# Kernel optimization log

Measured on AMD Instinct MI355X. Metric: run time of the kernel, lower is better.

## Reference

```python
import jax, jax.numpy as jnp
import numpy as np

N = 50000        # nodes
E = 800000       # edges (avg degree 16)
HID = 96         # hidden_channels
HEADS = 4        # heads passed to SRGATConv
D = HID // HEADS # per-head dim
R = 38           # num_relations
NEG_SLOPE = 0.2  # LeakyReLU slope for attention logits


def setup_inputs() -> dict:
    key = jax.random.key(0)
    ks = jax.random.split(key, 9)
    x = jax.random.normal(ks[0], (N, HID), jnp.float32)
    edge_index = jax.random.randint(ks[1], (2, E), 0, N, dtype=jnp.int32)
    edge_type = jax.random.randint(ks[2], (E,), 0, R, dtype=jnp.int32)
    s = 1.0 / np.sqrt(HID)
    W = jax.random.normal(ks[3], (HID, HID), jnp.float32) * s          # node projection
    rel_emb = jax.random.normal(ks[4], (R, HID), jnp.float32) * s      # relation embeddings
    att_src = jax.random.normal(ks[5], (HEADS, D), jnp.float32) * 0.1  # attention vectors
    att_dst = jax.random.normal(ks[6], (HEADS, D), jnp.float32) * 0.1
    att_rel = jax.random.normal(ks[7], (HEADS, D), jnp.float32) * 0.1
    bias = jnp.zeros((HID,), jnp.float32)
    return {"x": x, "edge_index": edge_index, "edge_type": edge_type,
            "W": W, "rel_emb": rel_emb, "att_src": att_src,
            "att_dst": att_dst, "att_rel": att_rel, "bias": bias}


def reference(x, edge_index, edge_type, W, rel_emb, att_src, att_dst, att_rel, bias):
    # SRGATConv: relation-aware multi-head graph attention, then GELU wrapper.
    n = x.shape[0]
    src, dst = edge_index[0], edge_index[1]
    h = (x @ W).reshape(n, HEADS, D)                    # [N,H,D]
    r = rel_emb[edge_type].reshape(-1, HEADS, D)        # [E,H,D] gathered relation feats
    h_src = h[src]                                      # [E,H,D] irregular gather
    h_dst = h[dst]
    # attention logits per edge/head
    logits = ((h_src * att_src).sum(-1)
              + (h_dst * att_dst).sum(-1)
              + (r * att_rel).sum(-1))                  # [E,H]
    logits = jax.nn.leaky_relu(logits, NEG_SLOPE)
    # segment softmax over incoming edges of each destination node
    lmax = jax.ops.segment_max(logits, dst, num_segments=n)   # [N,H]
    e = jnp.exp(logits - lmax[dst])
    denom = jax.ops.segment_sum(e, dst, num_segments=n)       # [N,H]
    alpha = e / denom[dst]                                    # [E,H]
    # weighted message scatter
    msg = alpha[:, :, None] * (h_src + r)                     # [E,H,D]
    out = jax.ops.segment_sum(msg, dst, num_segments=n).reshape(n, HID) + bias
    out = jax.nn.gelu(out)
    return out, alpha
```

## Files before the change

### kernel.cpp

```cpp
#include <hip/hip_runtime.h>
#include <hip/hip_fp16.h>
#include <math.h>

#define HIDC 96
#define HEADS 4
#define DH 24
#define RMAX 40
#define CAP 56
#define DEGS 8

__device__ __forceinline__ __half2 u2h2(unsigned u) {
    return *reinterpret_cast<__half2*>(&u);
}
__device__ __forceinline__ unsigned h22u(__half2 h) {
    return *reinterpret_cast<unsigned*>(&h);
}

__global__ __launch_bounds__(192) void gemm96(const float* __restrict__ x,
                                              const float* __restrict__ W,
                                              __half* __restrict__ h16,
                                              int* __restrict__ deg, int n) {
    for (int i = blockIdx.x * 192 + threadIdx.x; i < n * DEGS; i += gridDim.x * 192)
        deg[i] = 0;

    __shared__ float Ws[HIDC * HIDC];
    __shared__ float xs[32 * HIDC];
    for (int i = threadIdx.x; i < HIDC * HIDC / 4; i += 192)
        reinterpret_cast<float4*>(Ws)[i] = reinterpret_cast<const float4*>(W)[i];
    int c4 = threadIdx.x % 24;
    int r0 = (threadIdx.x / 24) * 4;
    const float4* xs4 = reinterpret_cast<const float4*>(xs);
    const float4* Ws4 = reinterpret_cast<const float4*>(Ws);
    uint2* h8 = reinterpret_cast<uint2*>(h16);
    int numTiles = (n + 31) >> 5;
    for (int tile = blockIdx.x; tile < numTiles; tile += gridDim.x) {
        int row0 = tile << 5;
        int rows = min(32, n - row0);
        __syncthreads();
        for (int i = threadIdx.x; i < rows * 24; i += 192)
            reinterpret_cast<float4*>(xs)[i] =
                reinterpret_cast<const float4*>(x + (size_t)row0 * HIDC)[i];
        __syncthreads();
        float4 acc[4];
#pragma unroll
        for (int i = 0; i < 4; ++i) acc[i] = make_float4(0.f, 0.f, 0.f, 0.f);
#pragma unroll 4
        for (int k4 = 0; k4 < 24; ++k4) {
            float4 xv[4], wv[4];
#pragma unroll
            for (int i = 0; i < 4; ++i) xv[i] = xs4[(r0 + i) * 24 + k4];
#pragma unroll
            for (int j = 0; j < 4; ++j) wv[j] = Ws4[(k4 * 4 + j) * 24 + c4];
#pragma unroll
            for (int i = 0; i < 4; ++i) {
                const float xi[4] = {xv[i].x, xv[i].y, xv[i].z, xv[i].w};
#pragma unroll
                for (int j = 0; j < 4; ++j) {
                    acc[i].x = fmaf(xi[j], wv[j].x, acc[i].x);
                    acc[i].y = fmaf(xi[j], wv[j].y, acc[i].y);
                    acc[i].z = fmaf(xi[j], wv[j].z, acc[i].z);
                    acc[i].w = fmaf(xi[j], wv[j].w, acc[i].w);
                }
            }
        }
#pragma unroll
        for (int i = 0; i < 4; ++i)
            if (r0 + i < rows) {
                __half2 lo = __floats2half2_rn(acc[i].x, acc[i].y);
                __half2 hi = __floats2half2_rn(acc[i].z, acc[i].w);
                uint2 pk;
                pk.x = h22u(lo);
                pk.y = h22u(hi);
                h8[(size_t)(row0 + r0 + i) * 24 + c4] = pk;
            }
    }
}

__global__ __launch_bounds__(256) void node_dots(
    const __half* __restrict__ h16,
    const float* __restrict__ att_src, const float* __restrict__ att_dst,
    const float* __restrict__ rel, const float* __restrict__ att_rel,
    float4* __restrict__ ps, float* __restrict__ pdi,
    float4* __restrict__ pr, int n, int R_) {
    if (blockIdx.x == gridDim.x - 1) {
        int t = threadIdx.x;
        if (t < R_) {
            const float4* rp = reinterpret_cast<const float4*>(rel + (size_t)t * HIDC);
            const float4* ar = reinterpret_cast<const float4*>(att_rel);
            float acc[HEADS] = {0, 0, 0, 0};
#pragma unroll
            for (int c = 0; c < 24; ++c) {
                float4 v = rp[c], a = ar[c];
                acc[c / 6] += v.x * a.x + v.y * a.y + v.z * a.z + v.w * a.w;
            }
            pr[t] = make_float4(acc[0], acc[1], acc[2], acc[3]);
        }
        return;
    }
    int i = blockIdx.x * blockDim.x + threadIdx.x;
    if (i >= n) return;
    const uint2* hp = reinterpret_cast<const uint2*>(h16 + (size_t)i * HIDC);
    const float4* as = reinterpret_cast<const float4*>(att_src);
    const float4* ad = reinterpret_cast<const float4*>(att_dst);
    float accs[HEADS] = {0, 0, 0, 0}, accd[HEADS] = {0, 0, 0, 0};
#pragma unroll
    for (int c = 0; c < 24; ++c) {
        uint2 hv = hp[c];
        float2 f0 = __half22float2(u2h2(hv.x));
        float2 f1 = __half22float2(u2h2(hv.y));
        float4 a = as[c], d = ad[c];
        int hh = c / 6;
        accs[hh] += f0.x * a.x + f0.y * a.y + f1.x * a.z + f1.y * a.w;
        accd[hh] += f0.x * d.x + f0.y * d.y + f1.x * d.z + f1.y * d.w;
    }
    ps[i] = make_float4(accs[0], accs[1], accs[2], accs[3]);
    *reinterpret_cast<float4*>(pdi + (size_t)i * 8) =
        make_float4(accd[0], accd[1], accd[2], accd[3]);
}

__device__ __forceinline__ float4 ev4(float4 a, float4 b, float4 c) {
    float l0 = a.x + b.x + c.x, l1 = a.y + b.y + c.y;
    float l2 = a.z + b.z + c.z, l3 = a.w + b.w + c.w;
    l0 = l0 >= 0.f ? l0 : 0.2f * l0;
    l1 = l1 >= 0.f ? l1 : 0.2f * l1;
    l2 = l2 >= 0.f ? l2 : 0.2f * l2;
    l3 = l3 >= 0.f ? l3 : 0.2f * l3;
    return make_float4(__expf(l0), __expf(l1), __expf(l2), __expf(l3));
}

__device__ __forceinline__ float gelu_f(float v) {
    float u = 0.7978845608028654f * (v + 0.044715f * v * v * v);
    u = fminf(fmaxf(u, -15.f), 15.f);
    float t = __expf(2.f * u);
    return 0.5f * v * (1.f + (t - 1.f) / (t + 1.f));
}

__global__ void fill_bucket(const int* __restrict__ src, const int* __restrict__ dst,
                            const int* __restrict__ et,
                            const float4* __restrict__ ps, const float* __restrict__ pdi,
                            const float4* __restrict__ pr,
                            int* __restrict__ deg, int4* __restrict__ bucket, int E_) {
    int e = blockIdx.x * blockDim.x + threadIdx.x;
    if (e >= E_) return;
    int d = dst[e];
    int pos = atomicAdd(&deg[(size_t)d * DEGS], 1);
    if (pos < CAP) {
        int s = src[e], t = et[e];
        float4 b = *reinterpret_cast<const float4*>(pdi + (size_t)d * 8);
        float4 v = ev4(ps[s], b, pr[t]);
        int4 pk;
        pk.x = s;
        pk.y = t;
        pk.z = (int)h22u(__floats2half2_rn(v.x, v.y));
        pk.w = (int)h22u(__floats2half2_rn(v.z, v.w));
        bucket[(size_t)d * CAP + pos] = pk;
    }
}

__global__ __launch_bounds__(256) void node_agg(
    const __half* __restrict__ h16, const float* __restrict__ rel,
    const int4* __restrict__ bucket, const int* __restrict__ deg,
    float* __restrict__ pdi, const float* __restrict__ bias,
    float* __restrict__ out, int n, int R_) {
    __shared__ unsigned short relh[RMAX * HIDC];
    for (int i = threadIdx.x; i < R_ * 24; i += 256) {
        float4 v = reinterpret_cast<const float4*>(rel)[i];
        uint2 pk;
        pk.x = h22u(__floats2half2_rn(v.x, v.y));
        pk.y = h22u(__floats2half2_rn(v.z, v.w));
        reinterpret_cast<uint2*>(relh)[i] = pk;
    }
    __syncthreads();

    int lane = threadIdx.x & 31;
    if (lane >= 24) return;
    const int j = lane;
    const int j4 = 4 * j;
    const int hh = j / 6;
    const float4 bv = *reinterpret_cast<const float4*>(bias + j4);
    const uint2* relr = reinterpret_cast<const uint2*>(relh);

    int hw0 = (blockIdx.x * blockDim.x + threadIdx.x) >> 5;
    int nHW = (gridDim.x * blockDim.x) >> 5;

    for (int hw = hw0; hw < n; hw += nHW) {
        int cnt = min(deg[(size_t)hw * DEGS], CAP);
        const int4* sp = bucket + (size_t)hw * CAP;
        float a0 = 0.f, a1 = 0.f, a2 = 0.f, a3 = 0.f;
        float dsum = 0.f;

        if (cnt > 0) {
            const int lim = cnt - 1;
            int4 pc[4];
#pragma unroll
            for (int u = 0; u < 4; ++u) pc[u] = sp[min(u, lim)];

            for (int k = 0; k < cnt; k += 4) {
                uint2 hv[4];
#pragma unroll
                for (int u = 0; u < 4; ++u)
                    hv[u] = *reinterpret_cast<const uint2*>(
                        h16 + (size_t)pc[u].x * HIDC + j4);
                int4 pn[4];
#pragma unroll
                for (int u = 0; u < 4; ++u) pn[u] = sp[min(k + 4 + u, lim)];
#pragma unroll
                for (int u = 0; u < 4; ++u) {
                    unsigned w = (hh & 2) ? (unsigned)pc[u].w : (unsigned)pc[u].z;
                    unsigned bits16 = (hh & 1) ? (w >> 16) : (w & 0xffffu);
                    float e = __half2float(__low2half(u2h2(bits16)));
                    e = (k + u < cnt) ? e : 0.f;
                    dsum += e;
                    uint2 rv = relr[pc[u].y * 24 + j];
                    float2 f01 = __half22float2(__hadd2(u2h2(hv[u].x), u2h2(rv.x)));
                    float2 f23 = __half22float2(__hadd2(u2h2(hv[u].y), u2h2(rv.y)));
                    a0 = fmaf(e, f01.x, a0);
                    a1 = fmaf(e, f01.y, a1);
                    a2 = fmaf(e, f23.x, a2);
                    a3 = fmaf(e, f23.y, a3);
                }
#pragma unroll
                for (int u = 0; u < 4; ++u) pc[u] = pn[u];
            }
        }
        float inv = dsum > 0.f ? 1.f / dsum : 0.f;
        if ((j % 6) == 0) pdi[(size_t)hw * 8 + 4 + hh] = inv;
        float4 o;
        o.x = gelu_f(a0 * inv + bv.x);
        o.y = gelu_f(a1 * inv + bv.y);
        o.z = gelu_f(a2 * inv + bv.z);
        o.w = gelu_f(a3 * inv + bv.w);
        *reinterpret_cast<float4*>(out + (size_t)hw * HIDC + j4) = o;
    }
}

__global__ void alpha_edge(const int* __restrict__ src, const int* __restrict__ dst,
                           const int* __restrict__ et,
                           const float4* __restrict__ ps, const float* __restrict__ pdi,
                           const float4* __restrict__ pr,
                           float4* __restrict__ alpha, int E_) {
    int e = blockIdx.x * blockDim.x + threadIdx.x;
    if (e >= E_) return;
    int d = dst[e];
    const float4* rec = reinterpret_cast<const float4*>(pdi + (size_t)d * 8);
    float4 b = rec[0];
    float4 iv = rec[1];
    float4 v = ev4(ps[src[e]], b, pr[et[e]]);
    alpha[e] = make_float4(v.x * iv.x, v.y * iv.y, v.z * iv.z, v.w * iv.w);
}

extern "C" void kernel_launch(void* const* d_in, const int* in_sizes, int n_in,
                              void* d_out, int out_size, void* d_ws, size_t ws_size,
                              hipStream_t stream) {
    const float* x       = (const float*)d_in[0];
    const int*   eidx    = (const int*)d_in[1];
    const int*   etype   = (const int*)d_in[2];
    const float* W       = (const float*)d_in[3];
    const float* rel     = (const float*)d_in[4];
    const float* att_src = (const float*)d_in[5];
    const float* att_dst = (const float*)d_in[6];
    const float* att_rel = (const float*)d_in[7];
    const float* bias    = (const float*)d_in[8];

    int N_ = in_sizes[0] / HIDC;
    int E_ = in_sizes[1] / 2;
    int R_ = in_sizes[4] / HIDC;
    const int* src  = eidx;
    const int* dstp = eidx + E_;

    char* ws = (char*)d_ws;
    __half* h16    = (__half*)ws;  ws += (size_t)N_ * HIDC * 2;
    float4* ps     = (float4*)ws;  ws += (size_t)N_ * 16;
    float*  pdi    = (float*)ws;   ws += (size_t)N_ * 32;
    float4* pr     = (float4*)ws;  ws += 1024;
    int*    deg    = (int*)ws;     ws += (size_t)N_ * DEGS * 4;
    int4*   bucket = (int4*)ws;    ws += (size_t)N_ * CAP * 16;

    float*  outv  = (float*)d_out;
    float4* alpha = (float4*)(outv + (size_t)N_ * HIDC);

    gemm96<<<(N_ + 31) / 32, 192, 0, stream>>>(x, W, h16, deg, N_);

    node_dots<<<(N_ + 255) / 256 + 1, 256, 0, stream>>>(
        h16, att_src, att_dst, rel, att_rel, ps, pdi, pr, N_, R_);

    fill_bucket<<<(E_ + 255) / 256, 256, 0, stream>>>(
        src, dstp, etype, ps, pdi, pr, deg, bucket, E_);

    node_agg<<<2048, 256, 0, stream>>>(
        h16, rel, bucket, deg, pdi, bias, outv, N_, R_);

    alpha_edge<<<(E_ + 255) / 256, 256, 0, stream>>>(
        src, dstp, etype, ps, pdi, pr, alpha, E_);
}
```

Baseline: 213.5 us.

## Fuse node dots with bucket fill and recompute edge logits in aggregation

```diff
diff --git a/kernel.cpp b/kernel.cpp
--- a/kernel.cpp
+++ b/kernel.cpp
@@ -6,8 +6,10 @@
 #define HEADS 4
 #define DH 24
 #define RMAX 40
-#define CAP 56
+#define CAP 64
 #define DEGS 8
+#define SRCB 18
+#define SRCM ((1 << SRCB) - 1)
 
 __device__ __forceinline__ __half2 u2h2(unsigned u) {
     return *reinterpret_cast<__half2*>(&u);
@@ -76,13 +78,37 @@
     }
 }
 
-__global__ __launch_bounds__(256) void node_dots(
+__global__ __launch_bounds__(256) void nd_fill(
     const __half* __restrict__ h16,
     const float* __restrict__ att_src, const float* __restrict__ att_dst,
     const float* __restrict__ rel, const float* __restrict__ att_rel,
-    float4* __restrict__ ps, float* __restrict__ pdi,
-    float4* __restrict__ pr, int n, int R_) {
-    if (blockIdx.x == gridDim.x - 1) {
+    float4* __restrict__ ps, float* __restrict__ pdi, float4* __restrict__ pr,
+    const int* __restrict__ src, const int* __restrict__ dst,
+    const int* __restrict__ et,
+    int* __restrict__ deg, int* __restrict__ bucket,
+    int n, int R_, int E_, int nB) {
+    int bid = blockIdx.x;
+    if (bid < nB) {
+        int i = bid * 256 + threadIdx.x;
+        if (i >= n) return;
+        const uint2* hp = reinterpret_cast<const uint2*>(h16 + (size_t)i * HIDC);
+        const float4* as = reinterpret_cast<const float4*>(att_src);
+        const float4* ad = reinterpret_cast<const float4*>(att_dst);
+        float accs[HEADS] = {0, 0, 0, 0}, accd[HEADS] = {0, 0, 0, 0};
+#pragma unroll
+        for (int c = 0; c < 24; ++c) {
+            uint2 hv = hp[c];
+            float2 f0 = __half22float2(u2h2(hv.x));
+            float2 f1 = __half22float2(u2h2(hv.y));
+            float4 a = as[c], d = ad[c];
+            int hh = c / 6;
+            accs[hh] += f0.x * a.x + f0.y * a.y + f1.x * a.z + f1.y * a.w;
+            accd[hh] += f0.x * d.x + f0.y * d.y + f1.x * d.z + f1.y * d.w;
+        }
+        ps[i] = make_float4(accs[0], accs[1], accs[2], accs[3]);
+        *reinterpret_cast<float4*>(pdi + (size_t)i * 8) =
+            make_float4(accd[0], accd[1], accd[2], accd[3]);
+    } else if (bid == nB) {
         int t = threadIdx.x;
         if (t < R_) {
             const float4* rp = reinterpret_cast<const float4*>(rel + (size_t)t * HIDC);
@@ -95,27 +121,14 @@
             }
             pr[t] = make_float4(acc[0], acc[1], acc[2], acc[3]);
         }
-        return;
-    }
-    int i = blockIdx.x * blockDim.x + threadIdx.x;
-    if (i >= n) return;
-    const uint2* hp = reinterpret_cast<const uint2*>(h16 + (size_t)i * HIDC);
-    const float4* as = reinterpret_cast<const float4*>(att_src);
-    const float4* ad = reinterpret_cast<const float4*>(att_dst);
-    float accs[HEADS] = {0, 0, 0, 0}, accd[HEADS] = {0, 0, 0, 0};
-#pragma unroll
-    for (int c = 0; c < 24; ++c) {
-        uint2 hv = hp[c];
-        float2 f0 = __half22float2(u2h2(hv.x));
-        float2 f1 = __half22float2(u2h2(hv.y));
-        float4 a = as[c], d = ad[c];
-        int hh = c / 6;
-        accs[hh] += f0.x * a.x + f0.y * a.y + f1.x * a.z + f1.y * a.w;
-        accd[hh] += f0.x * d.x + f0.y * d.y + f1.x * d.z + f1.y * d.w;
-    }
-    ps[i] = make_float4(accs[0], accs[1], accs[2], accs[3]);
-    *reinterpret_cast<float4*>(pdi + (size_t)i * 8) =
-        make_float4(accd[0], accd[1], accd[2], accd[3]);
+    } else {
+        int e = (bid - nB - 1) * 256 + threadIdx.x;
+        if (e >= E_) return;
+        int d = dst[e];
+        int pos = atomicAdd(&deg[(size_t)d * DEGS], 1);
+        if (pos < CAP)
+            bucket[(size_t)d * CAP + pos] = src[e] | (et[e] << SRCB);
+    }
 }
 
 __device__ __forceinline__ float4 ev4(float4 a, float4 b, float4 c) {
@@ -135,40 +148,25 @@
     return 0.5f * v * (1.f + (t - 1.f) / (t + 1.f));
 }
 
-__global__ void fill_bucket(const int* __restrict__ src, const int* __restrict__ dst,
-                            const int* __restrict__ et,
-                            const float4* __restrict__ ps, const float* __restrict__ pdi,
-                            const float4* __restrict__ pr,
-                            int* __restrict__ deg, int4* __restrict__ bucket, int E_) {
-    int e = blockIdx.x * blockDim.x + threadIdx.x;
-    if (e >= E_) return;
-    int d = dst[e];
-    int pos = atomicAdd(&deg[(size_t)d * DEGS], 1);
-    if (pos < CAP) {
-        int s = src[e], t = et[e];
-        float4 b = *reinterpret_cast<const float4*>(pdi + (size_t)d * 8);
-        float4 v = ev4(ps[s], b, pr[t]);
-        int4 pk;
-        pk.x = s;
-        pk.y = t;
-        pk.z = (int)h22u(__floats2half2_rn(v.x, v.y));
-        pk.w = (int)h22u(__floats2half2_rn(v.z, v.w));
-        bucket[(size_t)d * CAP + pos] = pk;
-    }
-}
-
 __global__ __launch_bounds__(256) void node_agg(
     const __half* __restrict__ h16, const float* __restrict__ rel,
-    const int4* __restrict__ bucket, const int* __restrict__ deg,
-    float* __restrict__ pdi, const float* __restrict__ bias,
+    const int* __restrict__ bucket, const int* __restrict__ deg,
+    const float* __restrict__ ps1, float* __restrict__ pdi,
+    const float4* __restrict__ prg, const float* __restrict__ bias,
     float* __restrict__ out, int n, int R_) {
     __shared__ unsigned short relh[RMAX * HIDC];
+    __shared__ float prs4[RMAX * 4];
     for (int i = threadIdx.x; i < R_ * 24; i += 256) {
         float4 v = reinterpret_cast<const float4*>(rel)[i];
         uint2 pk;
         pk.x = h22u(__floats2half2_rn(v.x, v.y));
         pk.y = h22u(__floats2half2_rn(v.z, v.w));
         reinterpret_cast<uint2*>(relh)[i] = pk;
+    }
+    for (int i = threadIdx.x; i < R_; i += 256) {
+        float4 v = prg[i];
+        prs4[4 * i + 0] = v.x; prs4[4 * i + 1] = v.y;
+        prs4[4 * i + 2] = v.z; prs4[4 * i + 3] = v.w;
     }
     __syncthreads();
 
@@ -185,33 +183,40 @@
 
     for (int hw = hw0; hw < n; hw += nHW) {
         int cnt = min(deg[(size_t)hw * DEGS], CAP);
-        const int4* sp = bucket + (size_t)hw * CAP;
+        const int* spw = bucket + (size_t)hw * CAP;
+        float pdh = pdi[(size_t)hw * 8 + hh];
         float a0 = 0.f, a1 = 0.f, a2 = 0.f, a3 = 0.f;
         float dsum = 0.f;
 
         if (cnt > 0) {
             const int lim = cnt - 1;
-            int4 pc[4];
-#pragma unroll
-            for (int u = 0; u < 4; ++u) pc[u] = sp[min(u, lim)];
+            int wc[4];
+#pragma unroll
+            for (int u = 0; u < 4; ++u) wc[u] = spw[min(u, lim)];
 
             for (int k = 0; k < cnt; k += 4) {
+                int s[4], t[4];
+#pragma unroll
+                for (int u = 0; u < 4; ++u) { s[u] = wc[u] & SRCM; t[u] = wc[u] >> SRCB; }
                 uint2 hv[4];
+                float pv[4];
 #pragma unroll
                 for (int u = 0; u < 4; ++u)
                     hv[u] = *reinterpret_cast<const uint2*>(
-                        h16 + (size_t)pc[u].x * HIDC + j4);
-                int4 pn[4];
-#pragma unroll
-                for (int u = 0; u < 4; ++u) pn[u] = sp[min(k + 4 + u, lim)];
+                        h16 + (size_t)s[u] * HIDC + j4);
+#pragma unroll
+                for (int u = 0; u < 4; ++u) pv[u] = ps1[(size_t)s[u] * 4 + hh];
+                int wn[4];
+#pragma unroll
+                for (int u = 0; u < 4; ++u) wn[u] = spw[min(k + 4 + u, lim)];
 #pragma unroll
                 for (int u = 0; u < 4; ++u) {
-                    unsigned w = (hh & 2) ? (unsigned)pc[u].w : (unsigned)pc[u].z;
-                    unsigned bits16 = (hh & 1) ? (w >> 16) : (w & 0xffffu);
-                    float e = __half2float(__low2half(u2h2(bits16)));
+                    float l = pv[u] + pdh + prs4[t[u] * 4 + hh];
+                    l = l >= 0.f ? l : 0.2f * l;
+                    float e = __expf(l);
                     e = (k + u < cnt) ? e : 0.f;
                     dsum += e;
-                    uint2 rv = relr[pc[u].y * 24 + j];
+                    uint2 rv = relr[t[u] * 24 + j];
                     float2 f01 = __half22float2(__hadd2(u2h2(hv[u].x), u2h2(rv.x)));
                     float2 f23 = __half22float2(__hadd2(u2h2(hv[u].y), u2h2(rv.y)));
                     a0 = fmaf(e, f01.x, a0);
@@ -220,7 +225,7 @@
                     a3 = fmaf(e, f23.y, a3);
                 }
 #pragma unroll
-                for (int u = 0; u < 4; ++u) pc[u] = pn[u];
+                for (int u = 0; u < 4; ++u) wc[u] = wn[u];
             }
         }
         float inv = dsum > 0.f ? 1.f / dsum : 0.f;
@@ -274,21 +279,21 @@
     float*  pdi    = (float*)ws;   ws += (size_t)N_ * 32;
     float4* pr     = (float4*)ws;  ws += 1024;
     int*    deg    = (int*)ws;     ws += (size_t)N_ * DEGS * 4;
-    int4*   bucket = (int4*)ws;    ws += (size_t)N_ * CAP * 16;
+    int*    bucket = (int*)ws;     ws += (size_t)N_ * CAP * 4;
 
     float*  outv  = (float*)d_out;
     float4* alpha = (float4*)(outv + (size_t)N_ * HIDC);
 
     gemm96<<<(N_ + 31) / 32, 192, 0, stream>>>(x, W, h16, deg, N_);
 
-    node_dots<<<(N_ + 255) / 256 + 1, 256, 0, stream>>>(
-        h16, att_src, att_dst, rel, att_rel, ps, pdi, pr, N_, R_);
-
-    fill_bucket<<<(E_ + 255) / 256, 256, 0, stream>>>(
-        src, dstp, etype, ps, pdi, pr, deg, bucket, E_);
+    int nB = (N_ + 255) / 256;
+    int eB = (E_ + 255) / 256;
+    nd_fill<<<nB + 1 + eB, 256, 0, stream>>>(
+        h16, att_src, att_dst, rel, att_rel, ps, pdi, pr,
+        src, dstp, etype, deg, bucket, N_, R_, E_, nB);
 
     node_agg<<<2048, 256, 0, stream>>>(
-        h16, rel, bucket, deg, pdi, bias, outv, N_, R_);
+        h16, rel, bucket, deg, (const float*)ps, pdi, pr, bias, outv, N_, R_);
 
     alpha_edge<<<(E_ + 255) / 256, 256, 0, stream>>>(
         src, dstp, etype, ps, pdi, pr, alpha, E_);
```

New measurement: 224.6 us. 5.2% more time.

## Replace per-node atomic bucket fill with two-pass binned counting sort into CSR

Applied to the files above, without the earlier changes.

```diff
diff --git a/kernel.cpp b/kernel.cpp
--- a/kernel.cpp
+++ b/kernel.cpp
@@ -4,10 +4,13 @@
 
 #define HIDC 96
 #define HEADS 4
-#define DH 24
 #define RMAX 40
-#define CAP 56
-#define DEGS 8
+#define BINSZ 128
+#define BINCAP 2560
+#define TILE 2048
+#define SRCB 18
+#define SRCM ((1 << SRCB) - 1)
+#define ETB 6
 
 __device__ __forceinline__ __half2 u2h2(unsigned u) {
     return *reinterpret_cast<__half2*>(&u);
@@ -19,9 +22,10 @@
 __global__ __launch_bounds__(192) void gemm96(const float* __restrict__ x,
                                               const float* __restrict__ W,
                                               __half* __restrict__ h16,
-                                              int* __restrict__ deg, int n) {
-    for (int i = blockIdx.x * 192 + threadIdx.x; i < n * DEGS; i += gridDim.x * 192)
-        deg[i] = 0;
+                                              int* __restrict__ bincnt,
+                                              int n, int nbins) {
+    for (int i = blockIdx.x * 192 + threadIdx.x; i < nbins; i += gridDim.x * 192)
+        bincnt[i] = 0;
 
     __shared__ float Ws[HIDC * HIDC];
     __shared__ float xs[32 * HIDC];
@@ -135,31 +139,120 @@
     return 0.5f * v * (1.f + (t - 1.f) / (t + 1.f));
 }
 
-__global__ void fill_bucket(const int* __restrict__ src, const int* __restrict__ dst,
-                            const int* __restrict__ et,
-                            const float4* __restrict__ ps, const float* __restrict__ pdi,
-                            const float4* __restrict__ pr,
-                            int* __restrict__ deg, int4* __restrict__ bucket, int E_) {
-    int e = blockIdx.x * blockDim.x + threadIdx.x;
-    if (e >= E_) return;
-    int d = dst[e];
-    int pos = atomicAdd(&deg[(size_t)d * DEGS], 1);
-    if (pos < CAP) {
-        int s = src[e], t = et[e];
-        float4 b = *reinterpret_cast<const float4*>(pdi + (size_t)d * 8);
-        float4 v = ev4(ps[s], b, pr[t]);
-        int4 pk;
-        pk.x = s;
-        pk.y = t;
-        pk.z = (int)h22u(__floats2half2_rn(v.x, v.y));
-        pk.w = (int)h22u(__floats2half2_rn(v.z, v.w));
-        bucket[(size_t)d * CAP + pos] = pk;
+__global__ __launch_bounds__(256) void bin_edges(
+    const int* __restrict__ src, const int* __restrict__ dst,
+    const int* __restrict__ et,
+    int* __restrict__ bincnt, int* __restrict__ binwords,
+    int E_, int nbins) {
+    __shared__ int hist[512];
+    __shared__ int base[512];
+    int e0 = blockIdx.x * TILE;
+    for (int i = threadIdx.x; i < nbins; i += 256) hist[i] = 0;
+    __syncthreads();
+    int mybin[8], myrank[8], myword[8];
+#pragma unroll
+    for (int u = 0; u < 8; ++u) {
+        int e = e0 + u * 256 + threadIdx.x;
+        mybin[u] = -1;
+        if (e < E_) {
+            int d = dst[e];
+            int b = d >> 7;
+            myword[u] = src[e] | (et[e] << SRCB) | ((d & (BINSZ - 1)) << (SRCB + ETB));
+            mybin[u] = b;
+            myrank[u] = atomicAdd(&hist[b], 1);
+        }
+    }
+    __syncthreads();
+    for (int i = threadIdx.x; i < nbins; i += 256)
+        base[i] = hist[i] > 0 ? atomicAdd(&bincnt[i], hist[i]) : 0;
+    __syncthreads();
+#pragma unroll
+    for (int u = 0; u < 8; ++u) {
+        if (mybin[u] >= 0) {
+            int pos = base[mybin[u]] + myrank[u];
+            if (pos < BINCAP)
+                binwords[(size_t)mybin[u] * BINCAP + pos] = myword[u];
+        }
+    }
+}
+
+__global__ __launch_bounds__(256) void bin_sort(
+    const int* __restrict__ bincnt, const int* __restrict__ binwords,
+    const float4* __restrict__ ps, const float* __restrict__ pdi,
+    const float4* __restrict__ prg,
+    int4* __restrict__ csr, int* __restrict__ noff, int* __restrict__ ncnt,
+    int n, int R_) {
+    __shared__ int cnts[BINSZ];
+    __shared__ int scanb[BINSZ];
+    __shared__ int nbase[BINSZ];
+    __shared__ float4 pdl[BINSZ];
+    __shared__ float4 prl[RMAX];
+    int bin = blockIdx.x;
+    int node0 = bin * BINSZ;
+    int total = min(bincnt[bin], BINCAP);
+
+    for (int i = threadIdx.x; i < BINSZ; i += 256) {
+        cnts[i] = 0;
+        int nd = node0 + i;
+        pdl[i] = (nd < n) ? *reinterpret_cast<const float4*>(pdi + (size_t)nd * 8)
+                          : make_float4(0.f, 0.f, 0.f, 0.f);
+    }
+    for (int i = threadIdx.x; i < R_; i += 256) prl[i] = prg[i];
+    __syncthreads();
+
+    int w[10], rk[10];
+#pragma unroll
+    for (int u = 0; u < 10; ++u) {
+        int k = u * 256 + threadIdx.x;
+        rk[u] = -1;
+        if (k < total) {
+            w[u] = binwords[(size_t)bin * BINCAP + k];
+            int dl = (w[u] >> (SRCB + ETB)) & (BINSZ - 1);
+            rk[u] = atomicAdd(&cnts[dl], 1);
+        }
+    }
+    __syncthreads();
+
+    if (threadIdx.x < BINSZ) scanb[threadIdx.x] = cnts[threadIdx.x];
+    __syncthreads();
+    for (int s = 1; s < BINSZ; s <<= 1) {
+        int v = 0;
+        if (threadIdx.x < BINSZ && threadIdx.x >= s) v = scanb[threadIdx.x - s];
+        __syncthreads();
+        if (threadIdx.x < BINSZ) scanb[threadIdx.x] += v;
+        __syncthreads();
+    }
+    if (threadIdx.x < BINSZ) {
+        nbase[threadIdx.x] = scanb[threadIdx.x] - cnts[threadIdx.x];
+        int nd = node0 + threadIdx.x;
+        if (nd < n) {
+            noff[nd] = bin * BINCAP + nbase[threadIdx.x];
+            ncnt[nd] = cnts[threadIdx.x];
+        }
+    }
+    __syncthreads();
+
+#pragma unroll
+    for (int u = 0; u < 10; ++u) {
+        if (rk[u] >= 0) {
+            int s = w[u] & SRCM;
+            int t = (w[u] >> SRCB) & ((1 << ETB) - 1);
+            int dl = (w[u] >> (SRCB + ETB)) & (BINSZ - 1);
+            float4 v = ev4(ps[s], pdl[dl], prl[t]);
+            int4 pk;
+            pk.x = s;
+            pk.y = t;
+            pk.z = (int)h22u(__floats2half2_rn(v.x, v.y));
+            pk.w = (int)h22u(__floats2half2_rn(v.z, v.w));
+            csr[(size_t)bin * BINCAP + nbase[dl] + rk[u]] = pk;
+        }
     }
 }
 
 __global__ __launch_bounds__(256) void node_agg(
     const __half* __restrict__ h16, const float* __restrict__ rel,
-    const int4* __restrict__ bucket, const int* __restrict__ deg,
+    const int4* __restrict__ csr, const int* __restrict__ noff,
+    const int* __restrict__ ncnt,
     float* __restrict__ pdi, const float* __restrict__ bias,
     float* __restrict__ out, int n, int R_) {
     __shared__ unsigned short relh[RMAX * HIDC];
@@ -184,8 +277,8 @@
     int nHW = (gridDim.x * blockDim.x) >> 5;
 
     for (int hw = hw0; hw < n; hw += nHW) {
-        int cnt = min(deg[(size_t)hw * DEGS], CAP);
-        const int4* sp = bucket + (size_t)hw * CAP;
+        int cnt = ncnt[hw];
+        const int4* sp = csr + noff[hw];
         float a0 = 0.f, a1 = 0.f, a2 = 0.f, a3 = 0.f;
         float dsum = 0.f;
 
@@ -267,28 +360,35 @@
     int R_ = in_sizes[4] / HIDC;
     const int* src  = eidx;
     const int* dstp = eidx + E_;
+    int nbins = (N_ + BINSZ - 1) / BINSZ;
 
     char* ws = (char*)d_ws;
-    __half* h16    = (__half*)ws;  ws += (size_t)N_ * HIDC * 2;
-    float4* ps     = (float4*)ws;  ws += (size_t)N_ * 16;
-    float*  pdi    = (float*)ws;   ws += (size_t)N_ * 32;
-    float4* pr     = (float4*)ws;  ws += 1024;
-    int*    deg    = (int*)ws;     ws += (size_t)N_ * DEGS * 4;
-    int4*   bucket = (int4*)ws;    ws += (size_t)N_ * CAP * 16;
+    __half* h16      = (__half*)ws; ws += (size_t)N_ * HIDC * 2;
+    float4* ps       = (float4*)ws; ws += (size_t)N_ * 16;
+    float*  pdi      = (float*)ws;  ws += (size_t)N_ * 32;
+    float4* pr       = (float4*)ws; ws += 1024;
+    int*    bincnt   = (int*)ws;    ws += (size_t)((nbins + 3) & ~3) * 4;
+    int*    noff     = (int*)ws;    ws += (size_t)((N_ + 3) & ~3) * 4;
+    int*    ncnt     = (int*)ws;    ws += (size_t)((N_ + 3) & ~3) * 4;
+    int*    binwords = (int*)ws;    ws += (size_t)nbins * BINCAP * 4;
+    int4*   csr      = (int4*)ws;   ws += (size_t)nbins * BINCAP * 16;
 
     float*  outv  = (float*)d_out;
     float4* alpha = (float4*)(outv + (size_t)N_ * HIDC);
 
-    gemm96<<<(N_ + 31) / 32, 192, 0, stream>>>(x, W, h16, deg, N_);
+    gemm96<<<(N_ + 31) / 32, 192, 0, stream>>>(x, W, h16, bincnt, N_, nbins);
 
     node_dots<<<(N_ + 255) / 256 + 1, 256, 0, stream>>>(
         h16, att_src, att_dst, rel, att_rel, ps, pdi, pr, N_, R_);
 
-    fill_bucket<<<(E_ + 255) / 256, 256, 0, stream>>>(
-        src, dstp, etype, ps, pdi, pr, deg, bucket, E_);
+    bin_edges<<<(E_ + TILE - 1) / TILE, 256, 0, stream>>>(
+        src, dstp, etype, bincnt, binwords, E_, nbins);
+
+    bin_sort<<<nbins, 256, 0, stream>>>(
+        bincnt, binwords, ps, pdi, pr, csr, noff, ncnt, N_, R_);
 
     node_agg<<<2048, 256, 0, stream>>>(
-        h16, rel, bucket, deg, pdi, bias, outv, N_, R_);
+        h16, rel, csr, noff, ncnt, pdi, bias, outv, N_, R_);
 
     alpha_edge<<<(E_ + 255) / 256, 256, 0, stream>>>(
         src, dstp, etype, ps, pdi, pr, alpha, E_);
```

Result: faster. 202.3 us (-5.2%).
